# Kernel optimization log

Measured on AMD Instinct MI355X. Metric: run time of the kernel, lower is better.

## Reference

```python
import jax, jax.numpy as jnp
import numpy as np

# Fixed by module source: forward hardcodes a 200x200 BEV grid, dim=128,
# MSDeformAttn(n_levels=1, n_heads=4, n_points=8).
B, Z, X, C, H, P = 2, 200, 200, 128, 4, 8
N = Z * X
D = C // H  # head dim = 32


def setup_inputs() -> dict:
    key = jax.random.key(0)
    ks = jax.random.split(key, 12)
    s = 0.02
    return {
        "query": jax.random.normal(ks[0], (B, N, C), jnp.float32),
        # MSDeformAttn.value_proj
        "Wv": jax.random.normal(ks[1], (C, C), jnp.float32) * s,
        "bv": jnp.zeros((C,), jnp.float32),
        # MSDeformAttn.sampling_offsets (C -> H*1*P*2)
        "Woff": jax.random.normal(ks[2], (C, H * P * 2), jnp.float32) * s,
        "boff": jax.random.normal(ks[3], (H * P * 2,), jnp.float32) * 2.0,
        # MSDeformAttn.attention_weights (C -> H*1*P)
        "Wattn": jax.random.normal(ks[4], (C, H * P), jnp.float32) * s,
        "battn": jnp.zeros((H * P,), jnp.float32),
        # MSDeformAttn.output_proj
        "Wout1": jax.random.normal(ks[5], (C, C), jnp.float32) * s,
        "bout1": jnp.zeros((C,), jnp.float32),
        # VanillaSelfAttention.output_proj
        "Wout2": jax.random.normal(ks[6], (C, C), jnp.float32) * s,
        "bout2": jnp.zeros((C,), jnp.float32),
    }


def _forward(query, Wv, bv, Woff, boff, Wattn, battn, Wout1, bout1, Wout2, bout2):
    # Reference points: normalized centers of the 200x200 grid, order (z, x).
    zc = (jnp.arange(Z, dtype=jnp.float32) + 0.5) / Z
    xc = (jnp.arange(X, dtype=jnp.float32) + 0.5) / X
    ref = jnp.stack(jnp.meshgrid(zc, xc, indexing="ij"), axis=-1).reshape(N, 2)

    # value_proj on input_flatten (== query); split heads, lay out as images.
    value = (query @ Wv + bv).reshape(B, Z, X, H, D)
    value_flat = value.transpose(0, 3, 1, 2, 4).reshape(B * H, Z * X, D)  # (BH, ZX, D)

    # Sampling locations: ref + offsets / offset_normalizer ([W, H] = [200, 200]).
    off = (query @ Woff + boff).reshape(B, N, H, P, 2)
    norm = jnp.array([X, Z], jnp.float32)
    loc = ref[None, :, None, None, :] + off / norm  # (B, N, H, P, 2)

    # Attention weights: softmax over n_levels*n_points (= P here).
    attn = jax.nn.softmax((query @ Wattn + battn).reshape(B, N, H, P), axis=-1)

    # grid_sample convention: grid = 2*loc - 1, grid[...,0]=x (width), align_corners=False.
    grid = 2.0 * loc - 1.0
    ix = ((grid[..., 0] + 1.0) * X - 1.0) * 0.5  # pixel x coords
    iy = ((grid[..., 1] + 1.0) * Z - 1.0) * 0.5  # pixel y coords
    ix = ix.transpose(0, 2, 1, 3).reshape(B * H, N * P)
    iy = iy.transpose(0, 2, 1, 3).reshape(B * H, N * P)

    x0f = jnp.floor(ix); y0f = jnp.floor(iy)
    lx = ix - x0f; ly = iy - y0f
    x0 = x0f.astype(jnp.int32); y0 = y0f.astype(jnp.int32)
    x1 = x0 + 1; y1 = y0 + 1

    def corner(xi, yi, w):
        # zero padding: out-of-bounds corners contribute 0
        valid = (xi >= 0) & (xi < X) & (yi >= 0) & (yi < Z)
        idx = jnp.clip(yi, 0, Z - 1) * X + jnp.clip(xi, 0, X - 1)  # (BH, N*P)
        v = jnp.take_along_axis(value_flat, idx[..., None], axis=1)  # (BH, N*P, D)
        return v * (w * valid.astype(w.dtype))[..., None]

    sampled = (
        corner(x0, y0, (1.0 - lx) * (1.0 - ly))
        + corner(x1, y0, lx * (1.0 - ly))
        + corner(x0, y1, (1.0 - lx) * ly)
        + corner(x1, y1, lx * ly)
    ).reshape(B, H, N, P, D)

    # Weighted reduce over points, merge heads.
    out = jnp.einsum("bhnpd,bnhp->bnhd", sampled, attn).reshape(B, N, C)
    out = out @ Wout1 + bout1  # MSDeformAttn.output_proj
    out = out @ Wout2 + bout2  # VanillaSelfAttention.output_proj
    return out + query  # dropout is identity in eval; residual add


def reference(query, Wv, bv, Woff, boff, Wattn, battn, Wout1, bout1, Wout2, bout2):
    return _forward(query, Wv, bv, Woff, boff, Wattn, battn, Wout1, bout1, Wout2, bout2)
```

## Files before the change

### kernel.cpp

```cpp
#include <hip/hip_runtime.h>
#include <hip/hip_bf16.h>
#include <cstddef>

namespace {
constexpr int B  = 2;
constexpr int Z  = 200;
constexpr int X  = 200;
constexpr int C  = 128;
constexpr int H  = 4;
constexpr int P  = 8;
constexpr int N  = Z * X;
constexpr int BN = B * N;
constexpr int SC = 96;
constexpr int NF_P = 14;
constexpr int NF_O = 8;
constexpr int KS   = 4;

typedef __attribute__((ext_vector_type(8))) short short8;
typedef __attribute__((ext_vector_type(4))) float f32x4;

__device__ inline ushort f2bf(float x) {
    __hip_bfloat16 h = __float2bfloat16(x);
    return *reinterpret_cast<ushort*>(&h);
}
__device__ inline float bflo(unsigned u) { return __uint_as_float(u << 16); }
__device__ inline float bfhi(unsigned u) { return __uint_as_float(u & 0xffff0000u); }
__device__ inline unsigned packbf(float a, float b) {
    return (unsigned)f2bf(a) | ((unsigned)f2bf(b) << 16);
}
template <int MASK>
__device__ inline float swzx(float x) {
    constexpr int pat = (MASK << 10) | 0x1F;
    return __int_as_float(__builtin_amdgcn_ds_swizzle(__float_as_int(x), pat));
}
}

__global__ __launch_bounds__(256) void vsa_k_prep(
    const float* __restrict__ Wv,    const float* __restrict__ bv,
    const float* __restrict__ Woff,  const float* __restrict__ boff,
    const float* __restrict__ Wattn, const float* __restrict__ battn,
    const float* __restrict__ Wout1, const float* __restrict__ bout1,
    const float* __restrict__ Wout2, const float* __restrict__ bout2,
    ushort* __restrict__ wtp, ushort* __restrict__ wtp2,
    float* __restrict__ biasp, float* __restrict__ bias2)
{
    const int u = blockIdx.x * 256 + threadIdx.x;
    constexpr int NP = KS * NF_P * 64;
    constexpr int NO = KS * NF_O * 64;

    if (u < NP) {
        int ks  = u / (NF_P * 64);
        int rem = u - ks * (NF_P * 64);
        int f = rem >> 6, l = rem & 63;
        int n  = f * 16 + (l & 15);
        int kb = ks * 32 + (l >> 4) * 8;
        float v[8];
        #pragma unroll
        for (int e = 0; e < 8; ++e) {
            int k = kb + e;
            if (n < 128)      v[e] = Wv[k * 128 + n];
            else if (n < 192) v[e] = Woff[k * 64 + (n - 128)];
            else              v[e] = Wattn[k * 32 + (n - 192)];
        }
        unsigned* dst = (unsigned*)(wtp + (size_t)u * 8);
        #pragma unroll
        for (int i = 0; i < 4; ++i) dst[i] = packbf(v[2*i], v[2*i+1]);
    } else if (u < NP + NO) {
        int t   = u - NP;
        int ks  = t / (NF_O * 64);
        int rem = t - ks * (NF_O * 64);
        int f = rem >> 6, l = rem & 63;
        int n  = f * 16 + (l & 15);
        int kb = ks * 32 + (l >> 4) * 8;
        float acc[8] = {0,0,0,0,0,0,0,0};
        for (int j = 0; j < 128; ++j) {
            float w2 = Wout2[j * 128 + n];
            #pragma unroll
            for (int e = 0; e < 8; ++e)
                acc[e] = fmaf(Wout1[(kb + e) * 128 + j], w2, acc[e]);
        }
        unsigned* dst = (unsigned*)(wtp2 + (size_t)t * 8);
        #pragma unroll
        for (int i = 0; i < 4; ++i) dst[i] = packbf(acc[2*i], acc[2*i+1]);
    } else if (u < NP + NO + 224) {
        int c = u - NP - NO;
        float bb;
        if (c < 128)      bb = bv[c];
        else if (c < 192) bb = boff[c - 128];
        else              bb = battn[c - 192];
        biasp[c] = bb;
    } else if (u < NP + NO + 224 + 128) {
        int c = u - NP - NO - 224;
        float acc = bout2[c];
        for (int j = 0; j < 128; ++j)
            acc = fmaf(bout1[j], Wout2[j * 128 + c], acc);
        bias2[c] = acc;
    }
}

__global__ __launch_bounds__(256) void vsa_k_proj(
    const float* __restrict__ Q, const ushort* __restrict__ wtp,
    const float* __restrict__ biasp,
    ushort* __restrict__ proj_v, float* __restrict__ proj_s)
{
    const int lane = threadIdx.x & 63;
    const int wave = blockIdx.x * 4 + (threadIdx.x >> 6);
    const int row0 = wave * 16;
    const int m  = lane & 15;
    const int kg = lane >> 4;

    const float* qp = Q + (size_t)(row0 + m) * 128 + kg * 8;

    f32x4 acc[NF_P];
    #pragma unroll
    for (int f = 0; f < NF_P; ++f) acc[f] = (f32x4){0.f, 0.f, 0.f, 0.f};

    #pragma unroll
    for (int ks = 0; ks < KS; ++ks) {
        float4 a0 = *(const float4*)(qp + ks * 32);
        float4 a1 = *(const float4*)(qp + ks * 32 + 4);
        short8 af;
        af[0] = (short)f2bf(a0.x); af[1] = (short)f2bf(a0.y);
        af[2] = (short)f2bf(a0.z); af[3] = (short)f2bf(a0.w);
        af[4] = (short)f2bf(a1.x); af[5] = (short)f2bf(a1.y);
        af[6] = (short)f2bf(a1.z); af[7] = (short)f2bf(a1.w);
        const short8* wrow = (const short8*)wtp + ks * NF_P * 64 + lane;
        #pragma unroll
        for (int f = 0; f < NF_P; ++f)
            acc[f] = __builtin_amdgcn_mfma_f32_16x16x32_bf16(af, wrow[f * 64], acc[f], 0, 0, 0);
    }

    #pragma unroll
    for (int f = 0; f < 8; ++f) {
        const int col = f * 16 + m;
        const float bb = biasp[col];
        #pragma unroll
        for (int r = 0; r < 4; ++r)
            proj_v[(size_t)(row0 + kg * 4 + r) * 128 + col] = f2bf(acc[f][r] + bb);
    }
    #pragma unroll
    for (int f = 8; f < 12; ++f) {
        const int col = f * 16 + m;
        const float bb = biasp[col];
        #pragma unroll
        for (int r = 0; r < 4; ++r)
            proj_s[(size_t)(row0 + kg * 4 + r) * SC + (col - 128)] = acc[f][r] + bb;
    }
    #pragma unroll
    for (int f = 12; f < 14; ++f) {
        const float bb = biasp[f * 16 + m];
        #pragma unroll
        for (int r = 0; r < 4; ++r) {
            float v = acc[f][r] + bb;
            float mx = v;
            mx = fmaxf(mx, swzx<1>(mx));
            mx = fmaxf(mx, swzx<2>(mx));
            mx = fmaxf(mx, swzx<4>(mx));
            float ex = __expf(v - mx);
            float sm = ex;
            sm += swzx<1>(sm); sm += swzx<2>(sm); sm += swzx<4>(sm);
            const float wp = ex / sm;
            proj_s[(size_t)(row0 + kg * 4 + r) * SC + 64 + (f - 12) * 16 + m] = wp;
        }
    }
}

__global__ __launch_bounds__(256) void vsa_k_sample(
    const ushort* __restrict__ proj_v, const float* __restrict__ proj_s,
    ushort* __restrict__ tmp)
{
    const int lane  = threadIdx.x & 63;
    const int w     = threadIdx.x >> 6;
    const int pixb  = w >> 1;
    const int hpair = w & 1;
    const int h     = hpair * 2 + (lane >> 5);
    const int p     = (lane >> 2) & 7;
    const int d8    = lane & 3;

    const int i = blockIdx.x * 2 + pixb;
    const int j = blockIdx.y;
    const int b = blockIdx.z;
    const int bn = b * N + i * X + j;

    const float* srow = proj_s + (size_t)bn * SC;
    const char*  vb   = (const char*)(proj_v + (size_t)b * N * 128);

    const float2 off = *(const float2*)(srow + (h * 8 + p) * 2);
    const float  wp  = srow[64 + h * 8 + p];

    const float ixf = (float)i + off.x;
    const float iyf = (float)j + off.y;
    const float x0f = floorf(ixf), y0f = floorf(iyf);
    const float lx = ixf - x0f, ly = iyf - y0f;
    const int x0 = (int)x0f, y0 = (int)y0f;
    const int x1 = x0 + 1,  y1 = y0 + 1;
    const int xc0 = min(max(x0, 0), X - 1), xc1 = min(max(x1, 0), X - 1);
    const int yc0 = min(max(y0, 0), Z - 1), yc1 = min(max(y1, 0), Z - 1);

    const float wx0 = ((unsigned)x0 < (unsigned)X) ? (1.f - lx) : 0.f;
    const float wx1 = ((unsigned)x1 < (unsigned)X) ? lx : 0.f;
    const float wy0 = (((unsigned)y0 < (unsigned)Z) ? (1.f - ly) : 0.f) * wp;
    const float wy1 = (((unsigned)y1 < (unsigned)Z) ? ly : 0.f) * wp;
    const float w00 = wx0 * wy0, w10 = wx1 * wy0;
    const float w01 = wx0 * wy1, w11 = wx1 * wy1;

    const int rb0 = yc0 * X, rb1 = yc1 * X;
    const int hb  = h * 64 + d8 * 16;

    const uint4 c00 = *(const uint4*)(vb + (rb0 + xc0) * 256 + hb);
    const uint4 c10 = *(const uint4*)(vb + (rb0 + xc1) * 256 + hb);
    const uint4 c01 = *(const uint4*)(vb + (rb1 + xc0) * 256 + hb);
    const uint4 c11 = *(const uint4*)(vb + (rb1 + xc1) * 256 + hb);

    float a0 = w00*bflo(c00.x) + w10*bflo(c10.x) + w01*bflo(c01.x) + w11*bflo(c11.x);
    float a1 = w00*bfhi(c00.x) + w10*bfhi(c10.x) + w01*bfhi(c01.x) + w11*bfhi(c11.x);
    float a2 = w00*bflo(c00.y) + w10*bflo(c10.y) + w01*bflo(c01.y) + w11*bflo(c11.y);
    float a3 = w00*bfhi(c00.y) + w10*bfhi(c10.y) + w01*bfhi(c01.y) + w11*bfhi(c11.y);
    float a4 = w00*bflo(c00.z) + w10*bflo(c10.z) + w01*bflo(c01.z) + w11*bflo(c11.z);
    float a5 = w00*bfhi(c00.z) + w10*bfhi(c10.z) + w01*bfhi(c01.z) + w11*bfhi(c11.z);
    float a6 = w00*bflo(c00.w) + w10*bflo(c10.w) + w01*bflo(c01.w) + w11*bflo(c11.w);
    float a7 = w00*bfhi(c00.w) + w10*bfhi(c10.w) + w01*bfhi(c01.w) + w11*bfhi(c11.w);

    a0 += swzx<4>(a0);  a1 += swzx<4>(a1);  a2 += swzx<4>(a2);  a3 += swzx<4>(a3);
    a4 += swzx<4>(a4);  a5 += swzx<4>(a5);  a6 += swzx<4>(a6);  a7 += swzx<4>(a7);
    a0 += swzx<8>(a0);  a1 += swzx<8>(a1);  a2 += swzx<8>(a2);  a3 += swzx<8>(a3);
    a4 += swzx<8>(a4);  a5 += swzx<8>(a5);  a6 += swzx<8>(a6);  a7 += swzx<8>(a7);
    a0 += swzx<16>(a0); a1 += swzx<16>(a1); a2 += swzx<16>(a2); a3 += swzx<16>(a3);
    a4 += swzx<16>(a4); a5 += swzx<16>(a5); a6 += swzx<16>(a6); a7 += swzx<16>(a7);

    if (p == 0) {
        uint4 o;
        o.x = packbf(a0, a1);
        o.y = packbf(a2, a3);
        o.z = packbf(a4, a5);
        o.w = packbf(a6, a7);
        *(uint4*)(tmp + bn * 128 + h * 32 + d8 * 8) = o;
    }
}

__global__ __launch_bounds__(256) void vsa_k_out(
    const ushort* __restrict__ tmp, const ushort* __restrict__ wtp2,
    const float* __restrict__ bias2, const float* __restrict__ Q,
    float* __restrict__ out)
{
    const int lane = threadIdx.x & 63;
    const int wave = blockIdx.x * 4 + (threadIdx.x >> 6);
    const int row0 = wave * 16;
    const int m  = lane & 15;
    const int kg = lane >> 4;

    const ushort* ap = tmp + (size_t)(row0 + m) * 128 + kg * 8;

    f32x4 acc[NF_O];
    #pragma unroll
    for (int f = 0; f < NF_O; ++f) acc[f] = (f32x4){0.f, 0.f, 0.f, 0.f};

    #pragma unroll
    for (int ks = 0; ks < KS; ++ks) {
        short8 af = *(const short8*)(ap + ks * 32);
        const short8* wrow = (const short8*)wtp2 + ks * NF_O * 64 + lane;
        #pragma unroll
        for (int f = 0; f < NF_O; ++f)
            acc[f] = __builtin_amdgcn_mfma_f32_16x16x32_bf16(af, wrow[f * 64], acc[f], 0, 0, 0);
    }

    #pragma unroll
    for (int f = 0; f < NF_O; ++f) {
        const int col = f * 16 + m;
        const float bb = bias2[col];
        #pragma unroll
        for (int r = 0; r < 4; ++r) {
            const int row = row0 + kg * 4 + r;
            out[(size_t)row * 128 + col] = acc[f][r] + bb + Q[(size_t)row * 128 + col];
        }
    }
}

extern "C" void kernel_launch(void* const* d_in, const int* in_sizes, int n_in,
                              void* d_out, int out_size, void* d_ws, size_t ws_size,
                              hipStream_t stream) {
    const float* Q     = (const float*)d_in[0];
    const float* Wv    = (const float*)d_in[1];
    const float* bv    = (const float*)d_in[2];
    const float* Woff  = (const float*)d_in[3];
    const float* boff  = (const float*)d_in[4];
    const float* Wattn = (const float*)d_in[5];
    const float* battn = (const float*)d_in[6];
    const float* Wout1 = (const float*)d_in[7];
    const float* bout1 = (const float*)d_in[8];
    const float* Wout2 = (const float*)d_in[9];
    const float* bout2 = (const float*)d_in[10];
    float* out = (float*)d_out;

    float*  proj_s = (float*)d_ws;
    float*  biasp  = proj_s + (size_t)BN * SC;
    float*  bias2  = biasp + 224;
    ushort* proj_v = (ushort*)(bias2 + 128);
    ushort* tmp    = proj_v + (size_t)BN * 128;
    ushort* wtp    = tmp + (size_t)BN * 128;
    ushort* wtp2   = wtp + (size_t)KS * NF_P * 64 * 8;

    constexpr int prep_n = KS * NF_P * 64 + KS * NF_O * 64 + 224 + 128;
    vsa_k_prep<<<(prep_n + 255) / 256, 256, 0, stream>>>(
        Wv, bv, Woff, boff, Wattn, battn, Wout1, bout1, Wout2, bout2,
        wtp, wtp2, biasp, bias2);
    vsa_k_proj<<<BN / 64, 256, 0, stream>>>(Q, wtp, biasp, proj_v, proj_s);
    vsa_k_sample<<<dim3(Z / 2, X, B), 256, 0, stream>>>(proj_v, proj_s, tmp);
    vsa_k_out<<<BN / 64, 256, 0, stream>>>(tmp, wtp2, bias2, Q, out);
}
```

Before: 102.4 us.

## Store value projection in fp8, sampling params in fp16, remap sample grid for XCDs

The value projection is now written as fp8 (e4m3) and read back with packed fp8-to-f32 conversions in the bilinear sampler, which halves the gather bytes per corner. Offsets and attention weights are stored as fp16 instead of fp32. The sample kernel moves to a 1D grid with a block-index remap that groups consecutive work across the 8 XCDs, so each XCD gets a contiguous slice of pixels and neighbouring gathers can hit its L2. The fp8 value storage costs accuracy, and fp16 offsets lose some precision in the sampling locations.

```diff
diff --git a/kernel.cpp b/kernel.cpp
--- a/kernel.cpp
+++ b/kernel.cpp
@@ -18,15 +18,26 @@
 
 typedef __attribute__((ext_vector_type(8))) short short8;
 typedef __attribute__((ext_vector_type(4))) float f32x4;
+typedef __attribute__((ext_vector_type(2))) float f32x2;
+typedef _Float16 h16x2 __attribute__((ext_vector_type(2)));
 
 __device__ inline ushort f2bf(float x) {
     __hip_bfloat16 h = __float2bfloat16(x);
     return *reinterpret_cast<ushort*>(&h);
 }
-__device__ inline float bflo(unsigned u) { return __uint_as_float(u << 16); }
-__device__ inline float bfhi(unsigned u) { return __uint_as_float(u & 0xffff0000u); }
 __device__ inline unsigned packbf(float a, float b) {
     return (unsigned)f2bf(a) | ((unsigned)f2bf(b) << 16);
+}
+__device__ inline ushort f2h(float x) {
+    _Float16 h = (_Float16)x;
+    return __builtin_bit_cast(ushort, h);
+}
+__device__ inline float h1f(ushort u) {
+    return (float)__builtin_bit_cast(_Float16, u);
+}
+__device__ inline float2 h2f2(unsigned u) {
+    h16x2 h = __builtin_bit_cast(h16x2, u);
+    return make_float2((float)h[0], (float)h[1]);
 }
 template <int MASK>
 __device__ inline float swzx(float x) {
@@ -101,7 +112,7 @@
 __global__ __launch_bounds__(256) void vsa_k_proj(
     const float* __restrict__ Q, const ushort* __restrict__ wtp,
     const float* __restrict__ biasp,
-    ushort* __restrict__ proj_v, float* __restrict__ proj_s)
+    unsigned char* __restrict__ proj_v8, ushort* __restrict__ proj_s16)
 {
     const int lane = threadIdx.x & 63;
     const int wave = blockIdx.x * 4 + (threadIdx.x >> 6);
@@ -135,8 +146,11 @@
         const int col = f * 16 + m;
         const float bb = biasp[col];
         #pragma unroll
-        for (int r = 0; r < 4; ++r)
-            proj_v[(size_t)(row0 + kg * 4 + r) * 128 + col] = f2bf(acc[f][r] + bb);
+        for (int r = 0; r < 4; ++r) {
+            const float v = acc[f][r] + bb;
+            const int pk = __builtin_amdgcn_cvt_pk_fp8_f32(v, v, 0, false);
+            proj_v8[(size_t)(row0 + kg * 4 + r) * 128 + col] = (unsigned char)pk;
+        }
     }
     #pragma unroll
     for (int f = 8; f < 12; ++f) {
@@ -144,7 +158,7 @@
         const float bb = biasp[col];
         #pragma unroll
         for (int r = 0; r < 4; ++r)
-            proj_s[(size_t)(row0 + kg * 4 + r) * SC + (col - 128)] = acc[f][r] + bb;
+            proj_s16[(size_t)(row0 + kg * 4 + r) * SC + (col - 128)] = f2h(acc[f][r] + bb);
     }
     #pragma unroll
     for (int f = 12; f < 14; ++f) {
@@ -160,13 +174,13 @@
             float sm = ex;
             sm += swzx<1>(sm); sm += swzx<2>(sm); sm += swzx<4>(sm);
             const float wp = ex / sm;
-            proj_s[(size_t)(row0 + kg * 4 + r) * SC + 64 + (f - 12) * 16 + m] = wp;
+            proj_s16[(size_t)(row0 + kg * 4 + r) * SC + 64 + (f - 12) * 16 + m] = f2h(wp);
         }
     }
 }
 
 __global__ __launch_bounds__(256) void vsa_k_sample(
-    const ushort* __restrict__ proj_v, const float* __restrict__ proj_s,
+    const unsigned char* __restrict__ proj_v8, const ushort* __restrict__ proj_s16,
     ushort* __restrict__ tmp)
 {
     const int lane  = threadIdx.x & 63;
@@ -177,16 +191,19 @@
     const int p     = (lane >> 2) & 7;
     const int d8    = lane & 3;
 
-    const int i = blockIdx.x * 2 + pixb;
-    const int j = blockIdx.y;
-    const int b = blockIdx.z;
-    const int bn = b * N + i * X + j;
-
-    const float* srow = proj_s + (size_t)bn * SC;
-    const char*  vb   = (const char*)(proj_v + (size_t)b * N * 128);
-
-    const float2 off = *(const float2*)(srow + (h * 8 + p) * 2);
-    const float  wp  = srow[64 + h * 8 + p];
+    const int orig = blockIdx.x;
+    const int wg   = (orig & 7) * 5000 + (orig >> 3);
+    const int b    = wg / 20000;
+    const int r2   = wg - b * 20000;
+    const int j    = r2 / 100;
+    const int i    = (r2 - j * 100) * 2 + pixb;
+    const int bn   = b * N + i * X + j;
+
+    const ushort* srow = proj_s16 + (size_t)bn * SC;
+    const unsigned char* vb = proj_v8 + (size_t)b * N * 128;
+
+    const float2 off = h2f2(*(const unsigned*)(srow + (h * 8 + p) * 2));
+    const float  wp  = h1f(srow[64 + h * 8 + p]);
 
     const float ixf = (float)i + off.x;
     const float iyf = (float)j + off.y;
@@ -205,21 +222,29 @@
     const float w01 = wx0 * wy1, w11 = wx1 * wy1;
 
     const int rb0 = yc0 * X, rb1 = yc1 * X;
-    const int hb  = h * 64 + d8 * 16;
-
-    const uint4 c00 = *(const uint4*)(vb + (rb0 + xc0) * 256 + hb);
-    const uint4 c10 = *(const uint4*)(vb + (rb0 + xc1) * 256 + hb);
-    const uint4 c01 = *(const uint4*)(vb + (rb1 + xc0) * 256 + hb);
-    const uint4 c11 = *(const uint4*)(vb + (rb1 + xc1) * 256 + hb);
-
-    float a0 = w00*bflo(c00.x) + w10*bflo(c10.x) + w01*bflo(c01.x) + w11*bflo(c11.x);
-    float a1 = w00*bfhi(c00.x) + w10*bfhi(c10.x) + w01*bfhi(c01.x) + w11*bfhi(c11.x);
-    float a2 = w00*bflo(c00.y) + w10*bflo(c10.y) + w01*bflo(c01.y) + w11*bflo(c11.y);
-    float a3 = w00*bfhi(c00.y) + w10*bfhi(c10.y) + w01*bfhi(c01.y) + w11*bfhi(c11.y);
-    float a4 = w00*bflo(c00.z) + w10*bflo(c10.z) + w01*bflo(c01.z) + w11*bflo(c11.z);
-    float a5 = w00*bfhi(c00.z) + w10*bfhi(c10.z) + w01*bfhi(c01.z) + w11*bfhi(c11.z);
-    float a6 = w00*bflo(c00.w) + w10*bflo(c10.w) + w01*bflo(c01.w) + w11*bflo(c11.w);
-    float a7 = w00*bfhi(c00.w) + w10*bfhi(c10.w) + w01*bfhi(c01.w) + w11*bfhi(c11.w);
+    const int hb  = h * 32 + d8 * 8;
+
+    const uint2 c00 = *(const uint2*)(vb + (rb0 + xc0) * 128 + hb);
+    const uint2 c10 = *(const uint2*)(vb + (rb0 + xc1) * 128 + hb);
+    const uint2 c01 = *(const uint2*)(vb + (rb1 + xc0) * 128 + hb);
+    const uint2 c11 = *(const uint2*)(vb + (rb1 + xc1) * 128 + hb);
+
+    float a0 = 0.f, a1 = 0.f, a2 = 0.f, a3 = 0.f;
+    float a4 = 0.f, a5 = 0.f, a6 = 0.f, a7 = 0.f;
+    #define VSA_ACC(c, wgt) { \
+        f32x2 u0 = __builtin_amdgcn_cvt_pk_f32_fp8((int)(c).x, false); \
+        f32x2 u1 = __builtin_amdgcn_cvt_pk_f32_fp8((int)(c).x, true);  \
+        f32x2 u2 = __builtin_amdgcn_cvt_pk_f32_fp8((int)(c).y, false); \
+        f32x2 u3 = __builtin_amdgcn_cvt_pk_f32_fp8((int)(c).y, true);  \
+        a0 = fmaf(wgt, u0.x, a0); a1 = fmaf(wgt, u0.y, a1); \
+        a2 = fmaf(wgt, u1.x, a2); a3 = fmaf(wgt, u1.y, a3); \
+        a4 = fmaf(wgt, u2.x, a4); a5 = fmaf(wgt, u2.y, a5); \
+        a6 = fmaf(wgt, u3.x, a6); a7 = fmaf(wgt, u3.y, a7); }
+    VSA_ACC(c00, w00)
+    VSA_ACC(c10, w10)
+    VSA_ACC(c01, w01)
+    VSA_ACC(c11, w11)
+    #undef VSA_ACC
 
     a0 += swzx<4>(a0);  a1 += swzx<4>(a1);  a2 += swzx<4>(a2);  a3 += swzx<4>(a3);
     a4 += swzx<4>(a4);  a5 += swzx<4>(a5);  a6 += swzx<4>(a6);  a7 += swzx<4>(a7);
@@ -234,7 +259,7 @@
         o.y = packbf(a2, a3);
         o.z = packbf(a4, a5);
         o.w = packbf(a6, a7);
-        *(uint4*)(tmp + bn * 128 + h * 32 + d8 * 8) = o;
+        *(uint4*)(tmp + (size_t)bn * 128 + h * 32 + d8 * 8) = o;
     }
 }
 
@@ -292,11 +317,11 @@
     const float* bout2 = (const float*)d_in[10];
     float* out = (float*)d_out;
 
-    float*  proj_s = (float*)d_ws;
-    float*  biasp  = proj_s + (size_t)BN * SC;
+    float*  biasp  = (float*)d_ws;
     float*  bias2  = biasp + 224;
-    ushort* proj_v = (ushort*)(bias2 + 128);
-    ushort* tmp    = proj_v + (size_t)BN * 128;
+    ushort* proj_s16 = (ushort*)(bias2 + 128);
+    unsigned char* proj_v8 = (unsigned char*)(proj_s16 + (size_t)BN * SC);
+    ushort* tmp    = (ushort*)(proj_v8 + (size_t)BN * 128);
     ushort* wtp    = tmp + (size_t)BN * 128;
     ushort* wtp2   = wtp + (size_t)KS * NF_P * 64 * 8;
 
@@ -304,7 +329,7 @@
     vsa_k_prep<<<(prep_n + 255) / 256, 256, 0, stream>>>(
         Wv, bv, Woff, boff, Wattn, battn, Wout1, bout1, Wout2, bout2,
         wtp, wtp2, biasp, bias2);
-    vsa_k_proj<<<BN / 64, 256, 0, stream>>>(Q, wtp, biasp, proj_v, proj_s);
-    vsa_k_sample<<<dim3(Z / 2, X, B), 256, 0, stream>>>(proj_v, proj_s, tmp);
+    vsa_k_proj<<<BN / 64, 256, 0, stream>>>(Q, wtp, biasp, proj_v8, proj_s16);
+    vsa_k_sample<<<dim3((Z / 2) * X * B), 256, 0, stream>>>(proj_v8, proj_s16, tmp);
     vsa_k_out<<<BN / 64, 256, 0, stream>>>(tmp, wtp2, bias2, Q, out);
 }
```

After: 98.54 us. -3.8%, faster.
